# Optimization experiments

Measured on AMD Instinct MI355X. Metric: run time of the kernel, lower is better.

Reference implementation:

```python
import jax, jax.numpy as jnp
import numpy as np

B, S, N, D = 32, 512, 64, 64


def setup_inputs() -> dict:
    key = jax.random.key(0)
    ks = jax.random.split(key, 6)
    return {
        "x": jax.random.normal(ks[0], (B, S, N, D), dtype=jnp.float32),
        "q_embed_weight": jax.random.normal(ks[1], (N, D), dtype=jnp.float32) * 0.02,
        "Wq_w": jax.random.normal(ks[2], (D, D), dtype=jnp.float32) * (1.0 / np.sqrt(D)),
        "Wq_b": jax.random.normal(ks[3], (D,), dtype=jnp.float32) * 0.02,
        "Wkv_w": jax.random.normal(ks[4], (2 * D, D), dtype=jnp.float32) * (1.0 / np.sqrt(D)),
        "Wkv_b": jax.random.normal(ks[5], (2 * D,), dtype=jnp.float32) * 0.02,
    }


def reference(x, q_embed_weight, Wq_w, Wq_b, Wkv_w, Wkv_b):
    d = x.shape[-1]
    # q = Wq(q_embed.weight): [n, d]
    q = q_embed_weight @ Wq_w.T + Wq_b
    # Wkv(x) -> [b, s, n, 2d]; chunk -> k is first half (v half is computed but unused, matching torch)
    kv = jnp.einsum('bsnd,ed->bsne', x, Wkv_w) + Wkv_b
    k = kv[..., :d]
    # prod: full contraction over n and d -> [b, s]
    prod = jnp.einsum('nd,bsnd->bs', q, k) / jnp.sqrt(jnp.asarray(d, x.dtype))
    attn = jax.nn.softmax(prod, axis=1)  # softmax over s
    # weighted sum over s with v = x (original overwrites v): [b, n, d]
    out = jnp.einsum('bs,bsnd->bnd', attn, x)
    return out
```

## Files before the change

kernel.cpp:

```cpp
#include <hip/hip_runtime.h>

#define B_   32
#define S_   512
#define ND_  4096
#define SCH  16
#define CH   32
#define RW   8
#define NUNIT (B_ * SCH)

typedef float f4 __attribute__((ext_vector_type(4)));

__global__ void qw_kernel(const float* __restrict__ qe, const float* __restrict__ Wq_w,
                          const float* __restrict__ Wq_b, const float* __restrict__ Wkv_w,
                          float* __restrict__ qw) {
    const int n = blockIdx.x;
    const int t = threadIdx.x;
    __shared__ float qrow[64];
    float acc = Wq_b[t];
    const float* qen = qe + n * 64;
    const float* wqr = Wq_w + t * 64;
#pragma unroll 8
    for (int d = 0; d < 64; ++d) acc += qen[d] * wqr[d];
    qrow[t] = acc;
    __syncthreads();
    float s = 0.f;
#pragma unroll 8
    for (int e = 0; e < 64; ++e) s += qrow[e] * Wkv_w[e * 64 + t];
    qw[n * 64 + t] = s * 0.125f;
}

__global__ __launch_bounds__(256, 2) void flash_partial(
    const float* __restrict__ x, const float* __restrict__ qw,
    float* __restrict__ po, float* __restrict__ pml) {
    const int blk = blockIdx.x;
    const int b   = blk >> 4;
    const int c   = blk & (SCH - 1);
    const int t   = threadIdx.x;
    const int w   = t >> 6;
    const int l   = t & 63;

    __shared__ f4 qws[1024];
    __shared__ f4 obuf[1024];
    __shared__ float slds[4];

#pragma unroll
    for (int k = 0; k < 4; ++k) qws[t + 256 * k] = ((const f4*)qw)[t + 256 * k];
    __syncthreads();

    f4 o[16];
#pragma unroll
    for (int j = 0; j < 16; ++j) o[j] = (f4)(0.f);
    float lsum = 0.f;

    const int s0 = c * CH + w * RW;
    const f4* xb = (const f4*)x + (size_t)(b * S_ + s0) * 1024;

#pragma unroll 2
    for (int r = 0; r < RW; ++r) {
        const f4* xr = xb + (size_t)r * 1024;
        f4 cur[16];
#pragma unroll
        for (int j = 0; j < 16; ++j) cur[j] = xr[j * 64 + l];

        int li = l;
        asm volatile("" : "+v"(li));
        float pd = 0.f;
#pragma unroll
        for (int j = 0; j < 16; ++j) {
            f4 qv = qws[j * 64 + li];
            pd += cur[j][0] * qv[0] + cur[j][1] * qv[1] +
                  cur[j][2] * qv[2] + cur[j][3] * qv[3];
        }
#pragma unroll
        for (int off = 32; off > 0; off >>= 1)
            pd += __shfl_xor(pd, off, 64);

        const float e = __expf(fminf(pd - 8.f, 52.f));
        lsum += e;
#pragma unroll
        for (int j = 0; j < 16; ++j) o[j] += e * cur[j];
    }

    if (l == 0) slds[w] = lsum;
    __syncthreads();
    const float L = slds[0] + slds[1] + slds[2] + slds[3];

    if (w == 0) {
#pragma unroll
        for (int j = 0; j < 16; ++j) obuf[j * 64 + l] = o[j];
    }
    __syncthreads();
#pragma unroll
    for (int ww = 1; ww < 4; ++ww) {
        if (w == ww) {
#pragma unroll
            for (int j = 0; j < 16; ++j) obuf[j * 64 + l] += o[j];
        }
        __syncthreads();
    }

    f4* pob = (f4*)po + (size_t)blk * 1024;
#pragma unroll
    for (int jj = 0; jj < 4; ++jj) {
        const int j = w * 4 + jj;
        pob[j * 64 + l] = obuf[j * 64 + l];
    }
    if (t == 0) pml[blk] = L;
}

__global__ __launch_bounds__(256) void combine_kernel(
    const float* __restrict__ po, const float* __restrict__ pml,
    float* __restrict__ out) {
    const int b   = blockIdx.x >> 4;
    const int seg = blockIdx.x & 15;
    const int t   = threadIdx.x;
    const int idx = seg * 256 + t;
    __shared__ float sl[SCH];
    if (t < SCH) sl[t] = pml[b * SCH + t];
    __syncthreads();
    float L = 0.f, acc = 0.f;
#pragma unroll
    for (int c = 0; c < SCH; ++c) {
        L   += sl[c];
        acc += po[(size_t)(b * SCH + c) * ND_ + idx];
    }
    out[(size_t)b * ND_ + idx] = acc / L;
}

extern "C" void kernel_launch(void* const* d_in, const int* in_sizes, int n_in,
                              void* d_out, int out_size, void* d_ws, size_t ws_size,
                              hipStream_t stream) {
    const float* x     = (const float*)d_in[0];
    const float* qe    = (const float*)d_in[1];
    const float* Wq_w  = (const float*)d_in[2];
    const float* Wq_b  = (const float*)d_in[3];
    const float* Wkv_w = (const float*)d_in[4];
    float* out = (float*)d_out;

    float* qw  = (float*)d_ws;
    float* pml = qw + ND_;
    float* po  = pml + NUNIT;

    qw_kernel<<<dim3(64), dim3(64), 0, stream>>>(qe, Wq_w, Wq_b, Wkv_w, qw);
    flash_partial<<<dim3(NUNIT), dim3(256), 0, stream>>>(x, qw, po, pml);
    combine_kernel<<<dim3(B_ * 16), dim3(256), 0, stream>>>(po, pml, out);
}
```

Measured before the change: 58.15 us.

## Split each x row across the whole block and reduce dot product via LDS barrier

```diff
diff --git a/kernel.cpp b/kernel.cpp
--- a/kernel.cpp
+++ b/kernel.cpp
@@ -1,11 +1,11 @@
 #include <hip/hip_runtime.h>
 
-#define B_   32
-#define S_   512
-#define ND_  4096
-#define SCH  16
-#define CH   32
-#define RW   8
+#define B_    32
+#define S_    512
+#define ND_   4096
+#define ND4_  1024
+#define SCH   16
+#define CH    32
 #define NUNIT (B_ * SCH)
 
 typedef float f4 __attribute__((ext_vector_type(4)));
@@ -29,7 +29,7 @@
     qw[n * 64 + t] = s * 0.125f;
 }
 
-__global__ __launch_bounds__(256, 2) void flash_partial(
+__global__ __launch_bounds__(256) void flash_partial(
     const float* __restrict__ x, const float* __restrict__ qw,
     float* __restrict__ po, float* __restrict__ pml) {
     const int blk = blockIdx.x;
@@ -39,73 +39,62 @@
     const int w   = t >> 6;
     const int l   = t & 63;
 
-    __shared__ f4 qws[1024];
-    __shared__ f4 obuf[1024];
-    __shared__ float slds[4];
+    __shared__ float red[2][4];
 
+    const f4* qw4 = (const f4*)qw;
+    f4 qv[4];
 #pragma unroll
-    for (int k = 0; k < 4; ++k) qws[t + 256 * k] = ((const f4*)qw)[t + 256 * k];
-    __syncthreads();
+    for (int k = 0; k < 4; ++k) qv[k] = qw4[k * 256 + t];
 
-    f4 o[16];
+    f4 o[4];
 #pragma unroll
-    for (int j = 0; j < 16; ++j) o[j] = (f4)(0.f);
+    for (int k = 0; k < 4; ++k) o[k] = (f4)(0.f);
     float lsum = 0.f;
 
-    const int s0 = c * CH + w * RW;
-    const f4* xb = (const f4*)x + (size_t)(b * S_ + s0) * 1024;
+    const f4* xb = (const f4*)x + (size_t)(b * S_ + c * CH) * ND4_;
 
-#pragma unroll 2
-    for (int r = 0; r < RW; ++r) {
-        const f4* xr = xb + (size_t)r * 1024;
-        f4 cur[16];
+    f4 cur[4], nxt[4];
 #pragma unroll
-        for (int j = 0; j < 16; ++j) cur[j] = xr[j * 64 + l];
+    for (int k = 0; k < 4; ++k) cur[k] = xb[k * 256 + t];
 
-        int li = l;
-        asm volatile("" : "+v"(li));
+    for (int si = 0; si < CH; ++si) {
+        if (si + 1 < CH) {
+            const f4* xn = xb + (size_t)(si + 1) * ND4_;
+#pragma unroll
+            for (int k = 0; k < 4; ++k) nxt[k] = xn[k * 256 + t];
+        }
+
         float pd = 0.f;
 #pragma unroll
-        for (int j = 0; j < 16; ++j) {
-            f4 qv = qws[j * 64 + li];
-            pd += cur[j][0] * qv[0] + cur[j][1] * qv[1] +
-                  cur[j][2] * qv[2] + cur[j][3] * qv[3];
-        }
+        for (int k = 0; k < 4; ++k)
+            pd += cur[k][0] * qv[k][0] + cur[k][1] * qv[k][1] +
+                  cur[k][2] * qv[k][2] + cur[k][3] * qv[k][3];
 #pragma unroll
         for (int off = 32; off > 0; off >>= 1)
             pd += __shfl_xor(pd, off, 64);
 
-        const float e = __expf(fminf(pd - 8.f, 52.f));
+        const int par = si & 1;
+        if (l == 0) red[par][w] = pd;
+        asm volatile("s_waitcnt lgkmcnt(0)" ::: "memory");
+        __builtin_amdgcn_s_barrier();
+        __builtin_amdgcn_sched_barrier(0);
+        const float p = red[par][0] + red[par][1] + red[par][2] + red[par][3];
+
+        const float e = __expf(fminf(p - 8.f, 52.f));
         lsum += e;
 #pragma unroll
-        for (int j = 0; j < 16; ++j) o[j] += e * cur[j];
+        for (int k = 0; k < 4; ++k) o[k] += e * cur[k];
+
+        if (si + 1 < CH) {
+#pragma unroll
+            for (int k = 0; k < 4; ++k) cur[k] = nxt[k];
+        }
     }
 
-    if (l == 0) slds[w] = lsum;
-    __syncthreads();
-    const float L = slds[0] + slds[1] + slds[2] + slds[3];
-
-    if (w == 0) {
+    f4* pob = (f4*)po + (size_t)blk * ND4_;
 #pragma unroll
-        for (int j = 0; j < 16; ++j) obuf[j * 64 + l] = o[j];
-    }
-    __syncthreads();
-#pragma unroll
-    for (int ww = 1; ww < 4; ++ww) {
-        if (w == ww) {
-#pragma unroll
-            for (int j = 0; j < 16; ++j) obuf[j * 64 + l] += o[j];
-        }
-        __syncthreads();
-    }
-
-    f4* pob = (f4*)po + (size_t)blk * 1024;
-#pragma unroll
-    for (int jj = 0; jj < 4; ++jj) {
-        const int j = w * 4 + jj;
-        pob[j * 64 + l] = obuf[j * 64 + l];
-    }
-    if (t == 0) pml[blk] = L;
+    for (int k = 0; k < 4; ++k) pob[k * 256 + t] = o[k];
+    if (t == 0) pml[blk] = lsum;
 }
 
 __global__ __launch_bounds__(256) void combine_kernel(
```

New measurement: 55.21 us. 1.05x faster.
